# Performance work log

Hardware: AMD Instinct MI355X
Metric: run time of the kernel (lower is better)

## Reference

```python
import jax, jax.numpy as jnp
import numpy as np

N = 8192
HID = 256
NCLS = 5
K = 10  # adj_parameter
IN_DIMS = [1000, 1000, 503]


def _leaky(x):
    return jnp.where(x >= 0, x, 0.25 * x)


def _batchnorm(x, g, b):
    # training-mode BatchNorm1d with batch stats (biased var), eps=1e-5
    mu = jnp.mean(x, axis=0)
    var = jnp.mean((x - mu) ** 2, axis=0)
    return (x - mu) * jax.lax.rsqrt(var + 1e-5) * g + b


def _build_adj(feat):
    # cosine similarity, per-row top-(K+1) (top-1 is self, diag=1), scatter,
    # add identity, L1 row-normalize. Vectorized equivalent of the torch loop.
    norm = jnp.maximum(jnp.linalg.norm(feat, axis=1, keepdims=True), 1e-12)
    fn = feat / norm
    sim = fn @ fn.T                                  # [N, N]
    vals, idx = jax.lax.top_k(sim, K + 1)            # [N, K+1]
    rows = jnp.arange(sim.shape[0])[:, None]
    adj = jnp.zeros_like(sim).at[rows, idx[:, 1:]].set(vals[:, 1:])
    adj = adj + jnp.eye(sim.shape[0], dtype=sim.dtype)
    rs = jnp.maximum(jnp.sum(jnp.abs(adj), axis=1, keepdims=True), 1e-12)
    return adj / rs


def setup_inputs() -> dict:
    key = jax.random.key(0)
    ks = jax.random.split(key, 24)
    d = {}
    d['x1'] = jax.random.normal(ks[0], (N, IN_DIMS[0]), jnp.float32)
    d['x2'] = jax.random.normal(ks[1], (N, IN_DIMS[1]), jnp.float32)
    d['x3'] = jax.random.normal(ks[2], (N, IN_DIMS[2]), jnp.float32)
    def xavier(k, shape):
        fan_in, fan_out = shape[-2], shape[-1]
        std = np.sqrt(2.0 / (fan_in + fan_out))
        return jax.random.normal(k, shape, jnp.float32) * std
    d['enc_W1'] = xavier(ks[3], (IN_DIMS[0], HID))
    d['enc_W2'] = xavier(ks[4], (IN_DIMS[1], HID))
    d['enc_W3'] = xavier(ks[5], (IN_DIMS[2], HID))
    d['enc_b'] = jnp.zeros((3, HID), jnp.float32)
    d['bn_g'] = jnp.ones((3, HID), jnp.float32)
    d['bn_b'] = jnp.zeros((3, HID), jnp.float32)
    d['gc1_W'] = xavier(ks[6], (3, HID, HID))
    d['gc1_b'] = jnp.zeros((3, HID), jnp.float32)
    d['gc2_W'] = xavier(ks[7], (3, HID, HID))
    d['gc2_b'] = jnp.zeros((3, HID), jnp.float32)
    d['clf_W'] = xavier(ks[8], (3, HID, NCLS))
    d['clf_b'] = jnp.zeros((3, NCLS), jnp.float32)
    d['attn'] = xavier(ks[9], (3, 1))[:, 0]
    d['f1_W'] = xavier(ks[10], (NCLS, 128))
    d['f1_b'] = jnp.zeros((128,), jnp.float32)
    d['f2_W'] = xavier(ks[11], (128, NCLS))
    d['f2_b'] = jnp.zeros((NCLS,), jnp.float32)
    return d


def reference(x1, x2, x3, enc_W1, enc_W2, enc_W3, enc_b, bn_g, bn_b,
              gc1_W, gc1_b, gc2_W, gc2_b, clf_W, clf_b,
              attn, f1_W, f1_b, f2_W, f2_b):
    xs = [x1, x2, x3]
    enc_Ws = [enc_W1, enc_W2, enc_W3]
    logits_list = []
    for i in range(3):
        # modal encoder: Linear -> ReLU -> BatchNorm (dropout off, eval)
        feat = jax.nn.relu(xs[i] @ enc_Ws[i] + enc_b[i])
        feat = _batchnorm(feat, bn_g[i], bn_b[i])
        adj = _build_adj(feat)
        # SimpleGCN: two GraphConvolution layers with leaky_relu(0.25)
        h = _leaky(adj @ (feat @ gc1_W[i]) + gc1_b[i])
        h = _leaky(adj @ (h @ gc2_W[i]) + gc2_b[i])
        logits_list.append(h @ clf_W[i] + clf_b[i])
    # SimpleVCDN fusion
    w = jax.nn.softmax(attn)
    fused = sum(w[i] * jax.nn.sigmoid(logits_list[i]) for i in range(3))
    out = _leaky(fused @ f1_W + f1_b) @ f2_W + f2_b
    return out
```

## Files before the change

kernel.cpp:

```cpp
#include <hip/hip_runtime.h>
#include <cfloat>
#include <cstdint>
#include <cstddef>

#define NROWS 8192
#define HID 256
#define NCLS 5
#define TOPK 10
#define CAP 256
#define TM 128
#define TN 128
#define BK 32
#define BKS 64

typedef __bf16 bf16x8 __attribute__((ext_vector_type(8)));
typedef float f32x4 __attribute__((ext_vector_type(4)));

__device__ inline ushort f2bf(float x) {
  unsigned u = __float_as_uint(x);
  unsigned r = (u + 0x7fffu + ((u >> 16) & 1u)) >> 16;
  return (ushort)r;
}
__device__ inline float bf2f(ushort b) { return __uint_as_float(((unsigned)b) << 16); }

__device__ __forceinline__ void load_lds16(const void* g, void* l) {
  __builtin_amdgcn_global_load_lds(
      (const __attribute__((address_space(1))) void*)g,
      (__attribute__((address_space(3))) void*)l, 16, 0, 0);
}

__global__ __launch_bounds__(256) void packAB_kernel(const float* __restrict__ X0,
    const float* __restrict__ X1, const float* __restrict__ X2,
    const float* __restrict__ W0, const float* __restrict__ W1,
    const float* __restrict__ W2, ushort* __restrict__ Ah, ushort* __restrict__ Al,
    ushort* __restrict__ Bh, ushort* __restrict__ Bl,
    int D0, int D1, int D2, int Kp0, int Kp1, int Kp2,
    size_t aOff0, size_t aOff1, size_t aOff2,
    size_t wOff0, size_t wOff1, size_t wOff2) {
  const int z = blockIdx.y;
  const float* X = (z == 0) ? X0 : (z == 1) ? X1 : X2;
  const float* W = (z == 0) ? W0 : (z == 1) ? W1 : W2;
  const int D = (z == 0) ? D0 : (z == 1) ? D1 : D2;
  const int Kp = (z == 0) ? Kp0 : (z == 1) ? Kp1 : Kp2;
  const size_t aOff = (z == 0) ? aOff0 : (z == 1) ? aOff1 : aOff2;
  const size_t wOff = (z == 0) ? wOff0 : (z == 1) ? wOff1 : wOff2;
  const int ksh = 31 - __clz(Kp);
  const int id = blockIdx.x * 256 + threadIdx.x;
  const int atotal = NROWS << ksh;
  if (id >= atotal + (HID << ksh)) return;
  if (id < atotal) {
    const int k = id & (Kp - 1);
    const int r = id >> ksh;
    const float x = (k < D) ? X[(size_t)r * D + k] : 0.f;
    const ushort h = f2bf(x);
    Ah[aOff + id] = h;
    Al[aOff + id] = f2bf(x - bf2f(h));
  } else {
    const int id2 = id - atotal;
    const int k = id2 & (Kp - 1);
    const int n = id2 >> ksh;
    const float x = (k < D) ? W[(size_t)k * HID + n] : 0.f;
    const ushort h = f2bf(x);
    Bh[wOff + id2] = h;
    Bl[wOff + id2] = f2bf(x - bf2f(h));
  }
}

__global__ __launch_bounds__(256) void packW_kernel(const float* __restrict__ W,
    ushort* __restrict__ Bh, ushort* __restrict__ Bl) {
  const int z = blockIdx.y;
  const int id = blockIdx.x * 256 + threadIdx.x;
  const int k = id >> 8, n = id & 255;
  const size_t wz = (size_t)z * HID * HID;
  const float x = W[wz + (size_t)k * HID + n];
  const ushort h = f2bf(x);
  Bh[wz + (size_t)n * HID + k] = h;
  Bl[wz + (size_t)n * HID + k] = f2bf(x - bf2f(h));
}

#define STAGE_LIMB(B, K0)                              \
    load_lds16(Ah + a0 + (K0), &AsH[B][p0 * 8]);       \
    load_lds16(Ah + a1 + (K0), &AsH[B][p1 * 8]);       \
    load_lds16(Al + a0 + (K0), &AsL[B][p0 * 8]);       \
    load_lds16(Al + a1 + (K0), &AsL[B][p1 * 8]);       \
    load_lds16(Bh + b0 + (K0), &BsH[B][p0 * 8]);       \
    load_lds16(Bh + b1 + (K0), &BsH[B][p1 * 8]);       \
    load_lds16(Bl + b0 + (K0), &BsL[B][p0 * 8]);       \
    load_lds16(Bl + b1 + (K0), &BsL[B][p1 * 8]);

template<bool BIAS, int ACT>
__global__ __launch_bounds__(256) void limbgemm_kernel(const ushort* __restrict__ Ah,
    const ushort* __restrict__ Al, const ushort* __restrict__ Bh,
    const ushort* __restrict__ Bl, const float* __restrict__ bias,
    float* __restrict__ C, int Kp0, int Kp1, int Kp2,
    size_t aOff0, size_t aOff1, size_t aOff2,
    size_t bOff0, size_t bOff1, size_t bOff2) {
  __shared__ ushort AsH[2][TM * BK], AsL[2][TM * BK], BsH[2][TM * BK], BsL[2][TM * BK];
  const int z = blockIdx.y;
  const int Kp = (z == 0) ? Kp0 : (z == 1) ? Kp1 : Kp2;
  const size_t aO = (z == 0) ? aOff0 : (z == 1) ? aOff1 : aOff2;
  const size_t bO = (z == 0) ? bOff0 : (z == 1) ? bOff1 : bOff2;
  Ah += aO; Al += aO; Bh += bO; Bl += bO;
  C += (size_t)z * NROWS * HID;
  const int tid = threadIdx.x;
  const int wave = tid >> 6, lane = tid & 63;
  const int bid = blockIdx.x;
  const int xcd = bid & 7, slot = bid >> 3;
  const int bxi = slot & 1;
  const int byi = xcd * 8 + (slot >> 1);
  const int bm = byi * TM, bn = bxi * 128;
  const int wr = (wave >> 1) * 64, wc = (wave & 1) * 64;

  f32x4 acc[4][4];
  const f32x4 zero = {0.f, 0.f, 0.f, 0.f};
  #pragma unroll
  for (int i = 0; i < 4; ++i)
    #pragma unroll
    for (int j = 0; j < 4; ++j) acc[i][j] = zero;

  const int p0 = tid, p1 = tid + 256;
  const int r0 = p0 >> 2, kl0 = (p0 & 3) ^ ((r0 & 3) ^ ((r0 >> 2) & 1));
  const int r1 = p1 >> 2, kl1 = (p1 & 3) ^ ((r1 & 3) ^ ((r1 >> 2) & 1));
  const size_t a0 = (size_t)(bm + r0) * Kp + kl0 * 8;
  const size_t a1 = (size_t)(bm + r1) * Kp + kl1 * 8;
  const size_t b0 = (size_t)(bn + r0) * Kp + kl0 * 8;
  const size_t b1 = (size_t)(bn + r1) * Kp + kl1 * 8;

  STAGE_LIMB(0, 0)
  __syncthreads();
  int cur = 0;
  for (int k0 = 0; k0 < Kp; k0 += BK) {
    if (k0 + BK < Kp) {
      STAGE_LIMB(cur ^ 1, k0 + BK)
    }
    bf16x8 ah[4], al[4], bh[4], bl[4];
    const int kg = lane >> 4;
    #pragma unroll
    for (int f = 0; f < 4; ++f) {
      const int m = wr + f * 16 + (lane & 15);
      const int sa = m * 4 + (kg ^ (m & 3) ^ ((m >> 2) & 1));
      ah[f] = *(const bf16x8*)&AsH[cur][sa * 8];
      al[f] = *(const bf16x8*)&AsL[cur][sa * 8];
      const int n = wc + f * 16 + (lane & 15);
      const int sb = n * 4 + (kg ^ (n & 3) ^ ((n >> 2) & 1));
      bh[f] = *(const bf16x8*)&BsH[cur][sb * 8];
      bl[f] = *(const bf16x8*)&BsL[cur][sb * 8];
    }
    #pragma unroll
    for (int fr = 0; fr < 4; ++fr)
      #pragma unroll
      for (int fc = 0; fc < 4; ++fc) {
        acc[fr][fc] = __builtin_amdgcn_mfma_f32_16x16x32_bf16(ah[fr], bh[fc], acc[fr][fc], 0, 0, 0);
        acc[fr][fc] = __builtin_amdgcn_mfma_f32_16x16x32_bf16(ah[fr], bl[fc], acc[fr][fc], 0, 0, 0);
        acc[fr][fc] = __builtin_amdgcn_mfma_f32_16x16x32_bf16(al[fr], bh[fc], acc[fr][fc], 0, 0, 0);
      }
    __syncthreads();
    cur ^= 1;
  }
  const int cq = lane >> 4, cc = lane & 15;
  #pragma unroll
  for (int fr = 0; fr < 4; ++fr) {
    #pragma unroll
    for (int fc = 0; fc < 4; ++fc) {
      const int rb = bm + wr + fr * 16 + cq * 4;
      const int col = bn + wc + fc * 16 + cc;
      const float bb = BIAS ? bias[z * HID + col] : 0.f;
      float* cp = C + (size_t)rb * HID + col;
      #pragma unroll
      for (int e = 0; e < 4; ++e) {
        float v = acc[fr][fc][e] + bb;
        if (ACT == 1) v = fmaxf(v, 0.f);
        cp[(size_t)e * HID] = v;
      }
    }
  }
}

__global__ __launch_bounds__(256) void bn_stats_kernel(const float* __restrict__ F,
    float* __restrict__ ps, float* __restrict__ ps2) {
  const int z = blockIdx.y;
  const int b = blockIdx.x, t = threadIdx.x;
  float s = 0.f, s2 = 0.f;
  const float* p = F + (size_t)z * NROWS * HID + (size_t)b * 128 * HID + t;
  for (int r = 0; r < 128; ++r) {
    const float v = p[(size_t)r * HID];
    s += v; s2 += v * v;
  }
  ps[(size_t)z * 64 * HID + b * HID + t] = s;
  ps2[(size_t)z * 64 * HID + b * HID + t] = s2;
}

__global__ __launch_bounds__(256) void bn_finalize_kernel(const float* __restrict__ ps,
    const float* __restrict__ ps2, const float* __restrict__ g,
    const float* __restrict__ b, float* __restrict__ scale, float* __restrict__ shift) {
  const int z = blockIdx.x;
  const int t = threadIdx.x;
  float s = 0.f, s2 = 0.f;
  for (int i = 0; i < 64; ++i) {
    s += ps[(size_t)z * 64 * HID + i * HID + t];
    s2 += ps2[(size_t)z * 64 * HID + i * HID + t];
  }
  const float mu = s / (float)NROWS;
  const float var = s2 / (float)NROWS - mu * mu;
  const float rstd = rsqrtf(var + 1e-5f);
  const float sc = rstd * g[z * HID + t];
  scale[z * HID + t] = sc;
  shift[z * HID + t] = b[z * HID + t] - mu * sc;
}

__global__ __launch_bounds__(256) void bn_rownorm_kernel(const float* __restrict__ F,
    const float* __restrict__ scale, const float* __restrict__ shift,
    float* __restrict__ FN, ushort* __restrict__ Ph,
    ushort* __restrict__ Fh, ushort* __restrict__ Fl) {
  const int z = blockIdx.y;
  const int r = blockIdx.x, t = threadIdx.x;
  const size_t zb = (size_t)z * NROWS * HID;
  const float f = F[zb + (size_t)r * HID + t] * scale[z * HID + t] + shift[z * HID + t];
  __shared__ float sh[256];
  sh[t] = f * f;
  __syncthreads();
  for (int st = 128; st > 0; st >>= 1) {
    if (t < st) sh[t] += sh[t + st];
    __syncthreads();
  }
  const float inv = 1.0f / fmaxf(sqrtf(sh[0]), 1e-12f);
  const float fn = f * inv;
  const size_t o = zb + (size_t)r * HID + t;
  FN[o] = fn;
  Ph[o] = f2bf(fn);
  const ushort h = f2bf(f);
  Fh[o] = h;
  Fl[o] = f2bf(f - bf2f(h));
}

template<int PASS>
__global__ __launch_bounds__(512) void simtile_kernel(const ushort* __restrict__ P,
    float* __restrict__ M, const float* __restrict__ tauv,
    int* __restrict__ gcnt, int* __restrict__ gidx) {
  const int tlin = blockIdx.x;
  int by = (int)(64.5f - sqrtf(4160.25f - 2.0f * (float)tlin));
  if (by < 0) by = 0;
  if (by > 63) by = 63;
  while (by > 0 && (by * 64 - (by * (by - 1)) / 2) > tlin) --by;
  while (by < 63 && ((by + 1) * 64 - ((by + 1) * by) / 2) <= tlin) ++by;
  const int bx = by + (tlin - (by * 64 - (by * (by - 1)) / 2));
  const int z = blockIdx.y;
  P += (size_t)z * NROWS * HID;
  if (PASS == 0) M += (size_t)z * NROWS * 64;
  else {
    tauv += (size_t)z * NROWS;
    gcnt += (size_t)z * NROWS;
    gidx += (size_t)z * NROWS * CAP;
  }
  const bool offdiag = (bx != by);
  __shared__ ushort As[TM * BKS];
  __shared__ ushort Bs[TN * BKS];
  __shared__ float Ml[2][TM];
  __shared__ float MlC[4][TN];
  __shared__ float taulA[TM];
  __shared__ float taulB[TN];
  const int tid = threadIdx.x;
  const int wave = tid >> 6, lane = tid & 63;
  const int bm = by * TM;
  const int bn = bx * TN;
  const int wr = (wave >> 1) * 32;
  const int wc = (wave & 1) * 64;

  if (PASS == 1) {
    if (tid < TM) taulA[tid] = tauv[bm + tid];
    else if (tid < TM + TN) taulB[tid - TM] = tauv[bn + (tid - TM)];
  }

  const ushort* pa[2];
  const ushort* pb[2];
  #pragma unroll
  for (int j = 0; j < 2; ++j) {
    const int s = tid + j * 512;
    const int m = s >> 3;
    const int kg = (s & 7) ^ (m & 7);
    pa[j] = P + (size_t)(bm + m) * HID + kg * 8;
    pb[j] = P + (size_t)(bn + m) * HID + kg * 8;
  }

  f32x4 acc[2][4];
  const f32x4 zero = {0.f, 0.f, 0.f, 0.f};
  #pragma unroll
  for (int i = 0; i < 2; ++i)
    #pragma unroll
    for (int j = 0; j < 4; ++j) acc[i][j] = zero;

  for (int k0 = 0; k0 < HID; k0 += BKS) {
    __syncthreads();
    #pragma unroll
    for (int j = 0; j < 2; ++j) {
      load_lds16(pa[j] + k0, &As[(tid + j * 512) * 8]);
      load_lds16(pb[j] + k0, &Bs[(tid + j * 512) * 8]);
    }
    __syncthreads();
    #pragma unroll
    for (int h = 0; h < 2; ++h) {
      const int kgb = h * 4 + (lane >> 4);
      bf16x8 af[2], bf[4];
      #pragma unroll
      for (int f = 0; f < 2; ++f) {
        const int m = wr + f * 16 + (lane & 15);
        const int sa = m * 8 + (kgb ^ (m & 7));
        af[f] = *(const bf16x8*)&As[sa * 8];
      }
      #pragma unroll
      for (int f = 0; f < 4; ++f) {
        const int n = wc + f * 16 + (lane & 15);
        const int sb = n * 8 + (kgb ^ (n & 7));
        bf[f] = *(const bf16x8*)&Bs[sb * 8];
      }
      #pragma unroll
      for (int fr = 0; fr < 2; ++fr)
        #pragma unroll
        for (int fc = 0; fc < 4; ++fc)
          acc[fr][fc] = __builtin_amdgcn_mfma_f32_16x16x32_bf16(af[fr], bf[fc], acc[fr][fc], 0, 0, 0);
    }
  }

  const int cq = lane >> 4, cc = lane & 15;
  if (PASS == 0) {
    #pragma unroll
    for (int fr = 0; fr < 2; ++fr) {
      #pragma unroll
      for (int e = 0; e < 4; ++e) {
        const int lrow = wr + fr * 16 + cq * 4 + e;
        const int grow = bm + lrow;
        float mx = -FLT_MAX;
        #pragma unroll
        for (int fc = 0; fc < 4; ++fc) {
          const int col = bn + wc + fc * 16 + cc;
          mx = fmaxf(mx, (col == grow) ? -FLT_MAX : acc[fr][fc][e]);
        }
        #pragma unroll
        for (int s = 1; s < 16; s <<= 1) mx = fmaxf(mx, __shfl_xor(mx, s));
        if (cc == 0) Ml[wave & 1][lrow] = mx;
      }
    }
    if (offdiag) {
      #pragma unroll
      for (int fc = 0; fc < 4; ++fc) {
        float mx = -FLT_MAX;
        #pragma unroll
        for (int fr = 0; fr < 2; ++fr)
          #pragma unroll
          for (int e = 0; e < 4; ++e) mx = fmaxf(mx, acc[fr][fc][e]);
        mx = fmaxf(mx, __shfl_xor(mx, 16));
        mx = fmaxf(mx, __shfl_xor(mx, 32));
        if (cq == 0) MlC[wave >> 1][wc + fc * 16 + cc] = mx;
      }
    }
    __syncthreads();
    if (tid < TM) M[(size_t)(bm + tid) * 64 + bx] = fmaxf(Ml[0][tid], Ml[1][tid]);
    if (offdiag && tid < TN) {
      const float mx = fmaxf(fmaxf(MlC[0][tid], MlC[1][tid]),
                             fmaxf(MlC[2][tid], MlC[3][tid]));
      M[(size_t)(bn + tid) * 64 + by] = mx;
    }
  } else {
    __syncthreads();
    #pragma unroll
    for (int fr = 0; fr < 2; ++fr) {
      #pragma unroll
      for (int e = 0; e < 4; ++e) {
        const int lrow = wr + fr * 16 + cq * 4 + e;
        const int grow = bm + lrow;
        const float tA = taulA[lrow];
        #pragma unroll
        for (int fc = 0; fc < 4; ++fc) {
          const int lcol = wc + fc * 16 + cc;
          const int gcol = bn + lcol;
          const float v = acc[fr][fc][e];
          if (gcol != grow && v >= tA) {
            const int pos = atomicAdd(&gcnt[grow], 1);
            if (pos < CAP) gidx[(size_t)grow * CAP + pos] = gcol;
          }
          if (offdiag && v >= taulB[lcol]) {
            const int pos = atomicAdd(&gcnt[gcol], 1);
            if (pos < CAP) gidx[(size_t)gcol * CAP + pos] = grow;
          }
        }
      }
    }
  }
}

__global__ __launch_bounds__(256) void tau_kernel(const float* __restrict__ M,
    float* __restrict__ tauv, int* __restrict__ gcnt) {
  const int z = blockIdx.y;
  const int wave = threadIdx.x >> 6, lane = threadIdx.x & 63;
  const int row = blockIdx.x * 4 + wave;
  float cur = M[(size_t)z * NROWS * 64 + (size_t)row * 64 + lane];
  float tau = cur;
  #pragma unroll
  for (int sel = 0; sel < 16; ++sel) {
    float bv = cur;
    int bl = lane;
    #pragma unroll
    for (int s = 1; s < 64; s <<= 1) {
      const float ov = __shfl_xor(bv, s);
      const int ol = __shfl_xor(bl, s);
      if (ov > bv || (ov == bv && ol < bl)) { bv = ov; bl = ol; }
    }
    tau = bv;
    if (lane == bl) cur = -FLT_MAX;
  }
  if (lane == 0) {
    tauv[(size_t)z * NROWS + row] = tau;
    gcnt[(size_t)z * NROWS + row] = 0;
  }
}

__global__ __launch_bounds__(256) void refine_kernel(const int* __restrict__ gcnt,
    const int* __restrict__ gidx, const float* __restrict__ FN,
    int* __restrict__ nidx, float* __restrict__ nval, float* __restrict__ dinv) {
  const int z = blockIdx.y;
  gcnt += (size_t)z * NROWS;
  gidx += (size_t)z * NROWS * CAP;
  FN += (size_t)z * NROWS * HID;
  nidx += (size_t)z * NROWS * TOPK;
  nval += (size_t)z * NROWS * TOPK;
  dinv += (size_t)z * NROWS;
  const int wave = threadIdx.x >> 6, lane = threadIdx.x & 63;
  const int row = blockIdx.x * 4 + wave;
  const int cnt = min(gcnt[row], CAP);
  __shared__ float fnrow[4][HID];
  __shared__ float ev[4][CAP];
  ((float4*)fnrow[wave])[lane] = ((const float4*)(FN + (size_t)row * HID))[lane];
  __syncthreads();
  const int c = lane >> 2, q4 = lane & 3;
  for (int b0 = 0; b0 < cnt; b0 += 16) {
    const int ci = b0 + c;
    const int cand = (ci < cnt) ? gidx[(size_t)row * CAP + ci] : 0;
    float s = 0.f;
    const float* fc = FN + (size_t)cand * HID + q4 * 64;
    const float* fr = fnrow[wave] + q4 * 64;
    #pragma unroll 8
    for (int k = 0; k < 64; ++k) s += fr[k] * fc[k];
    s += __shfl_xor(s, 1);
    s += __shfl_xor(s, 2);
    if (q4 == 0 && ci < cnt) ev[wave][ci] = s;
  }
  __syncthreads();
  float outv[TOPK];
  int outi[TOPK];
  float sum = 1.0f;
  #pragma unroll
  for (int sel = 0; sel < TOPK; ++sel) {
    float bv = -FLT_MAX;
    int bp = 0;
    #pragma unroll
    for (int j = 0; j < 4; ++j) {
      const int p = lane + j * 64;
      if (p < cnt) {
        const float v = ev[wave][p];
        if (v > bv) { bv = v; bp = p; }
      }
    }
    #pragma unroll
    for (int s = 1; s < 64; s <<= 1) {
      const float ov = __shfl_xor(bv, s);
      const int op = __shfl_xor(bp, s);
      if (ov > bv || (ov == bv && op < bp)) { bv = ov; bp = op; }
    }
    outv[sel] = bv;
    outi[sel] = bp;
    sum += fabsf(bv);
    if (lane == 0) ev[wave][bp] = -FLT_MAX;
  }
  if (lane == 0) {
    const float inv = 1.0f / fmaxf(sum, 1e-12f);
    dinv[row] = inv;
    #pragma unroll
    for (int sel = 0; sel < TOPK; ++sel) {
      nval[row * TOPK + sel] = outv[sel] * inv;
      nidx[row * TOPK + sel] = gidx[(size_t)row * CAP + outi[sel]];
    }
  }
}

template<int EMIT>
__global__ __launch_bounds__(256) void spmm_kernel(const float* __restrict__ T,
    const int* __restrict__ nidx, const float* __restrict__ nval,
    const float* __restrict__ dinv, const float* __restrict__ bias,
    ushort* __restrict__ Hh, ushort* __restrict__ Hl,
    const float* __restrict__ clfW, const float* __restrict__ clfb,
    float* __restrict__ L) {
  const int z = blockIdx.y;
  const size_t zb = (size_t)z * NROWS * HID;
  T += zb;
  nidx += (size_t)z * NROWS * TOPK;
  nval += (size_t)z * NROWS * TOPK;
  dinv += (size_t)z * NROWS;
  const int r = blockIdx.x, c = threadIdx.x;
  float acc = dinv[r] * T[(size_t)r * HID + c];
  #pragma unroll
  for (int n = 0; n < TOPK; ++n) {
    acc += nval[r * TOPK + n] * T[(size_t)nidx[r * TOPK + n] * HID + c];
  }
  acc += bias[z * HID + c];
  const float v = acc >= 0.f ? acc : 0.25f * acc;
  if (EMIT == 1) {
    const size_t o = zb + (size_t)r * HID + c;
    const ushort h = f2bf(v);
    Hh[o] = h;
    Hl[o] = f2bf(v - bf2f(h));
  } else {
    __shared__ float wsum[4][NCLS];
    const int wave = c >> 6, lane = c & 63;
    const float* wrow = clfW + (size_t)z * HID * NCLS + (size_t)c * NCLS;
    #pragma unroll
    for (int cls = 0; cls < NCLS; ++cls) {
      float p = v * wrow[cls];
      #pragma unroll
      for (int s = 1; s < 64; s <<= 1) p += __shfl_xor(p, s);
      if (lane == 0) wsum[wave][cls] = p;
    }
    __syncthreads();
    if (c < NCLS) {
      const float lg = clfb[z * NCLS + c] + wsum[0][c] + wsum[1][c] + wsum[2][c] + wsum[3][c];
      L[(size_t)z * NROWS * NCLS + (size_t)r * NCLS + c] = lg;
    }
  }
}

__global__ __launch_bounds__(256) void fuse_kernel(const float* __restrict__ L,
    const float* __restrict__ attn, float* __restrict__ fused) {
  const int id = blockIdx.x * 256 + threadIdx.x;
  if (id >= NROWS * NCLS) return;
  const float a0 = attn[0], a1 = attn[1], a2 = attn[2];
  const float m = fmaxf(a0, fmaxf(a1, a2));
  const float e0 = expf(a0 - m), e1 = expf(a1 - m), e2 = expf(a2 - m);
  const float inv = 1.0f / (e0 + e1 + e2);
  const float l0 = L[id];
  const float l1 = L[NROWS * NCLS + id];
  const float l2 = L[2 * NROWS * NCLS + id];
  const float s0 = 1.0f / (1.0f + expf(-l0));
  const float s1 = 1.0f / (1.0f + expf(-l1));
  const float s2 = 1.0f / (1.0f + expf(-l2));
  fused[id] = (e0 * s0 + e1 * s1 + e2 * s2) * inv;
}

__global__ __launch_bounds__(128) void head_kernel(const float* __restrict__ fused,
    const float* __restrict__ W1, const float* __restrict__ b1,
    const float* __restrict__ W2, const float* __restrict__ b2,
    float* __restrict__ out) {
  const int r = blockIdx.x, t = threadIdx.x;
  __shared__ float f[NCLS];
  __shared__ float hh[128];
  if (t < NCLS) f[t] = fused[r * NCLS + t];
  __syncthreads();
  float s = b1[t];
  #pragma unroll
  for (int k = 0; k < NCLS; ++k) s += f[k] * W1[k * 128 + t];
  hh[t] = s >= 0.f ? s : 0.25f * s;
  __syncthreads();
  if (t < NCLS) {
    float o = b2[t];
    for (int k = 0; k < 128; ++k) o += hh[k] * W2[k * NCLS + t];
    out[r * NCLS + t] = o;
  }
}

extern "C" void kernel_launch(void* const* d_in, const int* in_sizes, int n_in,
                              void* d_out, int out_size, void* d_ws, size_t ws_size,
                              hipStream_t stream) {
  const float* x0 = (const float*)d_in[0];
  const float* x1 = (const float*)d_in[1];
  const float* x2 = (const float*)d_in[2];
  const float* eW0 = (const float*)d_in[3];
  const float* eW1 = (const float*)d_in[4];
  const float* eW2 = (const float*)d_in[5];
  const float* enc_b = (const float*)d_in[6];
  const float* bn_g  = (const float*)d_in[7];
  const float* bn_b  = (const float*)d_in[8];
  const float* gc1W  = (const float*)d_in[9];
  const float* gc1b  = (const float*)d_in[10];
  const float* gc2W  = (const float*)d_in[11];
  const float* gc2b  = (const float*)d_in[12];
  const float* clfW  = (const float*)d_in[13];
  const float* clfb  = (const float*)d_in[14];
  const float* attn  = (const float*)d_in[15];
  const float* f1W   = (const float*)d_in[16];
  const float* f1b   = (const float*)d_in[17];
  const float* f2W   = (const float*)d_in[18];
  const float* f2b   = (const float*)d_in[19];
  float* out = (float*)d_out;

  int Kp[3];
  for (int m = 0; m < 3; ++m) {
    const int D = in_sizes[m] / NROWS;
    int k = 256;
    while (k < D) k <<= 1;
    Kp[m] = k;
  }
  const size_t KpSum = (size_t)Kp[0] + Kp[1] + Kp[2];
  const int D0 = in_sizes[0] / NROWS, D1 = in_sizes[1] / NROWS, D2 = in_sizes[2] / NROWS;

  const size_t NH = (size_t)NROWS * HID;
  float* ws = (float*)d_ws;
  float* A = ws;
  float* C = A;
  float* nval = A + 3 * NH;
  int*   nidx = (int*)(nval + (size_t)3 * NROWS * TOPK);
  float* dinv = (float*)(nidx + (size_t)3 * NROWS * TOPK);
  float* logits = dinv + 3 * NROWS;
  float* fused = logits + (size_t)3 * NROWS * NCLS;
  float* ps    = fused + (size_t)NROWS * NCLS;
  float* ps2   = ps + 3 * 64 * HID;
  float* scale = ps2 + 3 * 64 * HID;
  float* shift = scale + 3 * HID;
  float* M     = shift + 3 * HID;
  float* tauv  = M + (size_t)3 * NROWS * 64;
  int*   gcnt  = (int*)(tauv + 3 * NROWS);
  int*   gidx  = gcnt + 3 * NROWS;
  ushort* WhG = (ushort*)(gidx + (size_t)3 * NROWS * CAP);
  ushort* WlG = WhG + (size_t)3 * HID * HID;
  ushort* WhE = WlG + (size_t)3 * HID * HID;
  ushort* WlE = WhE + (size_t)HID * KpSum;
  char* u3 = (char*)(WlE + (size_t)HID * KpSum);
  float* FN = (float*)u3;
  ushort* Ph = (ushort*)(FN + 3 * NH);
  ushort* Fh = Ph + 3 * NH;
  ushort* Fl = Fh + 3 * NH;
  ushort* Hh = Fl + 3 * NH;
  ushort* Hl = Hh + 3 * NH;
  ushort* AhE = (ushort*)u3;
  ushort* AlE = AhE + (size_t)NROWS * KpSum;

  const size_t aOff0 = 0, aOff1 = (size_t)NROWS * Kp[0],
               aOff2 = (size_t)NROWS * (Kp[0] + Kp[1]);
  const size_t wOff0 = 0, wOff1 = (size_t)HID * Kp[0],
               wOff2 = (size_t)HID * (Kp[0] + Kp[1]);

  const dim3 blk(256);
  packAB_kernel<<<dim3(((NROWS + HID) * 1024) / 256, 3), blk, 0, stream>>>(
      x0, x1, x2, eW0, eW1, eW2, AhE, AlE, WhE, WlE,
      D0, D1, D2, Kp[0], Kp[1], Kp[2], aOff0, aOff1, aOff2, wOff0, wOff1, wOff2);
  limbgemm_kernel<true, 1><<<dim3(128, 3), blk, 0, stream>>>(
      AhE, AlE, WhE, WlE, enc_b, A, Kp[0], Kp[1], Kp[2],
      aOff0, aOff1, aOff2, wOff0, wOff1, wOff2);
  bn_stats_kernel<<<dim3(64, 3), blk, 0, stream>>>(A, ps, ps2);
  bn_finalize_kernel<<<3, blk, 0, stream>>>(ps, ps2, bn_g, bn_b, scale, shift);
  bn_rownorm_kernel<<<dim3(NROWS, 3), blk, 0, stream>>>(A, scale, shift, FN, Ph, Fh, Fl);
  simtile_kernel<0><<<dim3(2080, 3), dim3(512), 0, stream>>>(Ph, M, nullptr, nullptr, nullptr);
  tau_kernel<<<dim3(NROWS / 4, 3), blk, 0, stream>>>(M, tauv, gcnt);
  simtile_kernel<1><<<dim3(2080, 3), dim3(512), 0, stream>>>(Ph, nullptr, tauv, gcnt, gidx);
  refine_kernel<<<dim3(NROWS / 4, 3), blk, 0, stream>>>(gcnt, gidx, FN, nidx, nval, dinv);
  packW_kernel<<<dim3(256, 3), blk, 0, stream>>>(gc1W, WhG, WlG);
  limbgemm_kernel<false, 0><<<dim3(128, 3), blk, 0, stream>>>(
      Fh, Fl, WhG, WlG, nullptr, C, HID, HID, HID,
      0, NH, 2 * NH, 0, (size_t)HID * HID, (size_t)2 * HID * HID);
  spmm_kernel<1><<<dim3(NROWS, 3), blk, 0, stream>>>(C, nidx, nval, dinv, gc1b,
                                                     Hh, Hl, nullptr, nullptr, nullptr);
  packW_kernel<<<dim3(256, 3), blk, 0, stream>>>(gc2W, WhG, WlG);
  limbgemm_kernel<false, 0><<<dim3(128, 3), blk, 0, stream>>>(
      Hh, Hl, WhG, WlG, nullptr, C, HID, HID, HID,
      0, NH, 2 * NH, 0, (size_t)HID * HID, (size_t)2 * HID * HID);
  spmm_kernel<0><<<dim3(NROWS, 3), blk, 0, stream>>>(C, nidx, nval, dinv, gc2b,
                                                     nullptr, nullptr, clfW, clfb, logits);
  fuse_kernel<<<(NROWS * NCLS + 255) / 256, blk, 0, stream>>>(logits, attn, fused);
  head_kernel<<<NROWS, dim3(128), 0, stream>>>(fused, f1W, f1b, f2W, f2b, out);
}
```

Before: 748.9 us.

## Double-buffer simtile LDS loads and vectorize packAB input conversion

After: 754.3 us. Within noise of the previous version (+0.7%).

```diff
diff --git a/kernel.cpp b/kernel.cpp
--- a/kernel.cpp
+++ b/kernel.cpp
@@ -11,10 +11,10 @@
 #define TM 128
 #define TN 128
 #define BK 32
-#define BKS 64
 
 typedef __bf16 bf16x8 __attribute__((ext_vector_type(8)));
 typedef float f32x4 __attribute__((ext_vector_type(4)));
+typedef unsigned short us4 __attribute__((ext_vector_type(4)));
 
 __device__ inline ushort f2bf(float x) {
   unsigned u = __float_as_uint(x);
@@ -44,25 +44,43 @@
   const int Kp = (z == 0) ? Kp0 : (z == 1) ? Kp1 : Kp2;
   const size_t aOff = (z == 0) ? aOff0 : (z == 1) ? aOff1 : aOff2;
   const size_t wOff = (z == 0) ? wOff0 : (z == 1) ? wOff1 : wOff2;
-  const int ksh = 31 - __clz(Kp);
-  const int id = blockIdx.x * 256 + threadIdx.x;
-  const int atotal = NROWS << ksh;
-  if (id >= atotal + (HID << ksh)) return;
-  if (id < atotal) {
-    const int k = id & (Kp - 1);
-    const int r = id >> ksh;
-    const float x = (k < D) ? X[(size_t)r * D + k] : 0.f;
-    const ushort h = f2bf(x);
-    Ah[aOff + id] = h;
-    Al[aOff + id] = f2bf(x - bf2f(h));
+  const int ksh2 = (31 - __clz(Kp)) - 2;
+  const int id4 = blockIdx.x * 256 + threadIdx.x;
+  const int aq = NROWS << ksh2;
+  const int wq = HID << ksh2;
+  if (id4 >= aq + wq) return;
+  float x[4];
+  ushort h[4], l[4];
+  if (id4 < aq) {
+    const int kq = id4 & ((Kp >> 2) - 1);
+    const int r = id4 >> ksh2;
+    const int k = kq << 2;
+    const float* src = X + (size_t)r * D + k;
+    if (k + 3 < D && ((((size_t)r * D + k) & 3) == 0)) {
+      const float4 v = *(const float4*)src;
+      x[0] = v.x; x[1] = v.y; x[2] = v.z; x[3] = v.w;
+    } else {
+      #pragma unroll
+      for (int j = 0; j < 4; ++j) x[j] = (k + j < D) ? src[j] : 0.f;
+    }
+    #pragma unroll
+    for (int j = 0; j < 4; ++j) { h[j] = f2bf(x[j]); l[j] = f2bf(x[j] - bf2f(h[j])); }
+    const size_t o = aOff + (((size_t)r) << (ksh2 + 2)) + k;
+    *(us4*)&Ah[o] = (us4){h[0], h[1], h[2], h[3]};
+    *(us4*)&Al[o] = (us4){l[0], l[1], l[2], l[3]};
   } else {
-    const int id2 = id - atotal;
-    const int k = id2 & (Kp - 1);
-    const int n = id2 >> ksh;
-    const float x = (k < D) ? W[(size_t)k * HID + n] : 0.f;
-    const ushort h = f2bf(x);
-    Bh[wOff + id2] = h;
-    Bl[wOff + id2] = f2bf(x - bf2f(h));
+    const int id2 = id4 - aq;
+    const int kq = id2 & ((Kp >> 2) - 1);
+    const int n = id2 >> ksh2;
+    const int k = kq << 2;
+    #pragma unroll
+    for (int j = 0; j < 4; ++j) {
+      const float xv = (k + j < D) ? W[(size_t)(k + j) * HID + n] : 0.f;
+      h[j] = f2bf(xv); l[j] = f2bf(xv - bf2f(h[j]));
+    }
+    const size_t o = wOff + (((size_t)n) << (ksh2 + 2)) + k;
+    *(us4*)&Bh[o] = (us4){h[0], h[1], h[2], h[3]};
+    *(us4*)&Bl[o] = (us4){l[0], l[1], l[2], l[3]};
   }
 }
 
@@ -253,8 +271,8 @@
     gidx += (size_t)z * NROWS * CAP;
   }
   const bool offdiag = (bx != by);
-  __shared__ ushort As[TM * BKS];
-  __shared__ ushort Bs[TN * BKS];
+  __shared__ ushort As[2][TM * 32];
+  __shared__ ushort Bs[2][TN * 32];
   __shared__ float Ml[2][TM];
   __shared__ float MlC[4][TN];
   __shared__ float taulA[TM];
@@ -271,16 +289,10 @@
     else if (tid < TM + TN) taulB[tid - TM] = tauv[bn + (tid - TM)];
   }
 
-  const ushort* pa[2];
-  const ushort* pb[2];
-  #pragma unroll
-  for (int j = 0; j < 2; ++j) {
-    const int s = tid + j * 512;
-    const int m = s >> 3;
-    const int kg = (s & 7) ^ (m & 7);
-    pa[j] = P + (size_t)(bm + m) * HID + kg * 8;
-    pb[j] = P + (size_t)(bn + m) * HID + kg * 8;
-  }
+  const int sm = tid >> 2;
+  const int skl = (tid & 3) ^ ((sm & 3) ^ ((sm >> 2) & 1));
+  const ushort* pa = P + (size_t)(bm + sm) * HID + skl * 8;
+  const ushort* pb = P + (size_t)(bn + sm) * HID + skl * 8;
 
   f32x4 acc[2][4];
   const f32x4 zero = {0.f, 0.f, 0.f, 0.f};
@@ -289,36 +301,36 @@
     #pragma unroll
     for (int j = 0; j < 4; ++j) acc[i][j] = zero;
 
-  for (int k0 = 0; k0 < HID; k0 += BKS) {
+  load_lds16(pa, &As[0][tid * 8]);
+  load_lds16(pb, &Bs[0][tid * 8]);
+  __syncthreads();
+  int cur = 0;
+  for (int k0 = 0; k0 < HID; k0 += 32) {
+    if (k0 + 32 < HID) {
+      load_lds16(pa + k0 + 32, &As[cur ^ 1][tid * 8]);
+      load_lds16(pb + k0 + 32, &Bs[cur ^ 1][tid * 8]);
+    }
+    const int kg = lane >> 4;
+    bf16x8 af[2], bf[4];
+    #pragma unroll
+    for (int f = 0; f < 2; ++f) {
+      const int m = wr + f * 16 + (lane & 15);
+      const int sa = m * 4 + (kg ^ (m & 3) ^ ((m >> 2) & 1));
+      af[f] = *(const bf16x8*)&As[cur][sa * 8];
+    }
+    #pragma unroll
+    for (int f = 0; f < 4; ++f) {
+      const int n = wc + f * 16 + (lane & 15);
+      const int sb = n * 4 + (kg ^ (n & 3) ^ ((n >> 2) & 1));
+      bf[f] = *(const bf16x8*)&Bs[cur][sb * 8];
+    }
+    #pragma unroll
+    for (int fr = 0; fr < 2; ++fr)
+      #pragma unroll
+      for (int fc = 0; fc < 4; ++fc)
+        acc[fr][fc] = __builtin_amdgcn_mfma_f32_16x16x32_bf16(af[fr], bf[fc], acc[fr][fc], 0, 0, 0);
     __syncthreads();
-    #pragma unroll
-    for (int j = 0; j < 2; ++j) {
-      load_lds16(pa[j] + k0, &As[(tid + j * 512) * 8]);
-      load_lds16(pb[j] + k0, &Bs[(tid + j * 512) * 8]);
-    }
-    __syncthreads();
-    #pragma unroll
-    for (int h = 0; h < 2; ++h) {
-      const int kgb = h * 4 + (lane >> 4);
-      bf16x8 af[2], bf[4];
-      #pragma unroll
-      for (int f = 0; f < 2; ++f) {
-        const int m = wr + f * 16 + (lane & 15);
-        const int sa = m * 8 + (kgb ^ (m & 7));
-        af[f] = *(const bf16x8*)&As[sa * 8];
-      }
-      #pragma unroll
-      for (int f = 0; f < 4; ++f) {
-        const int n = wc + f * 16 + (lane & 15);
-        const int sb = n * 8 + (kgb ^ (n & 7));
-        bf[f] = *(const bf16x8*)&Bs[sb * 8];
-      }
-      #pragma unroll
-      for (int fr = 0; fr < 2; ++fr)
-        #pragma unroll
-        for (int fc = 0; fc < 4; ++fc)
-          acc[fr][fc] = __builtin_amdgcn_mfma_f32_16x16x32_bf16(af[fr], bf[fc], acc[fr][fc], 0, 0, 0);
-    }
+    cur ^= 1;
   }
 
   const int cq = lane >> 4, cc = lane & 15;
@@ -637,7 +649,7 @@
                wOff2 = (size_t)HID * (Kp[0] + Kp[1]);
 
   const dim3 blk(256);
-  packAB_kernel<<<dim3(((NROWS + HID) * 1024) / 256, 3), blk, 0, stream>>>(
+  packAB_kernel<<<dim3(((NROWS + HID) * 1024 / 4) / 256, 3), blk, 0, stream>>>(
       x0, x1, x2, eW0, eW1, eW2, AhE, AlE, WhE, WlE,
       D0, D1, D2, Kp[0], Kp[1], Kp[2], aOff0, aOff1, aOff2, wOff0, wOff1, wOff2);
   limbgemm_kernel<true, 1><<<dim3(128, 3), blk, 0, stream>>>(
```
